# Kernel tuning notes

Hardware: AMD Instinct MI355X
Metric: run time of the kernel (lower is better)

Reference implementation:

```python
import jax, jax.numpy as jnp
import numpy as np

B, H, S, D = 2, 16, 1024, 64

def setup_inputs() -> dict:
    key = jax.random.key(0)
    k1, k2 = jax.random.split(key)
    # x1 is the output of a softmax (attention probabilities): non-negative, rows sum to 1
    logits = jax.random.normal(k1, (B, H, S, S), dtype=jnp.float32)
    x1 = jax.nn.softmax(logits, axis=-1)
    x2 = jax.random.normal(k2, (B, H, S, D), dtype=jnp.float32)
    return {"x1": x1, "x2": x2}

def reference(x1, x2):
    # Forward of EfficientMemoryGEMMWithSoftmax: exact batched GEMM.
    # (The outlier/low-bit compression only affects what is cached for backward;
    #  the forward output is the exact product.)
    return jnp.einsum('bhsk,bhkd->bhsd', x1, x2)
```

## Files before the change

kernel.cpp:

```cpp
#include <hip/hip_runtime.h>
#include <hip/hip_bf16.h>

typedef __attribute__((ext_vector_type(8))) short short8_t;
typedef __attribute__((ext_vector_type(4))) short short4_t;
typedef __attribute__((ext_vector_type(4))) float f32x4;

#define S_DIM   1024
#define D_DIM   64
#define BM      128
#define KC      64
#define NCHUNK  (S_DIM / KC)
#define BSTRIDE 72
#define THREADS 512

__device__ __forceinline__ ushort f2bf(float f) {
    __hip_bfloat16 h = __float2bfloat16(f);
    return __builtin_bit_cast(ushort, h);
}

#define SYNC() do { \
    __builtin_amdgcn_sched_barrier(0); \
    asm volatile("s_waitcnt lgkmcnt(0)"); \
    __builtin_amdgcn_s_barrier(); \
    __builtin_amdgcn_sched_barrier(0); \
} while (0)

__global__ __launch_bounds__(THREADS, 1)
void gemm_sm_kernel(const float* __restrict__ x1,
                    const float* __restrict__ x2,
                    float* __restrict__ out) {
    __shared__ ushort lds_b[2][D_DIM * BSTRIDE];

    const int tid = threadIdx.x;
    const int bid = blockIdx.x;
    const int batch   = (bid & 7) * 4 + (bid >> 6);
    const int rowtile = (bid >> 3) & 7;
    const int row0    = rowtile * BM;

    const float* Abase = x1 + (size_t)batch * (S_DIM * S_DIM) + (size_t)row0 * S_DIM;
    const float* Bbase = x2 + (size_t)batch * (S_DIM * D_DIM);
    float*       Cbase = out + (size_t)batch * (S_DIM * D_DIM) + (size_t)row0 * D_DIM;

    const int w = tid >> 6;
    const int l = tid & 63;
    const int fr = l & 15, fg = l >> 4;

    const float* arow = Abase + (size_t)(w * 16 + fr) * S_DIM + fg * 8;

    const int bd  = l;
    const int bk0 = w * 4;

    int bidx[4][2];
    #pragma unroll
    for (int nf = 0; nf < 4; ++nf) {
        const int col = nf * 16 + fr;
        #pragma unroll
        for (int ks = 0; ks < 2; ++ks)
            bidx[nf][ks] = col * BSTRIDE + ks * 32 + fg * 8;
    }

    float a0[16], a1[16], b0[8], b1[8];

    auto loadA = [&](int t, float (&A)[16]) {
        #pragma unroll
        for (int ks = 0; ks < 2; ++ks) {
            const float* p = arow + t * KC + ks * 32;
            float4 v0 = *reinterpret_cast<const float4*>(p);
            float4 v1 = *reinterpret_cast<const float4*>(p + 4);
            A[ks * 8 + 0] = v0.x; A[ks * 8 + 1] = v0.y;
            A[ks * 8 + 2] = v0.z; A[ks * 8 + 3] = v0.w;
            A[ks * 8 + 4] = v1.x; A[ks * 8 + 5] = v1.y;
            A[ks * 8 + 6] = v1.z; A[ks * 8 + 7] = v1.w;
        }
    };
    auto loadB = [&](int t, float (&B)[8]) {
        const float* bp = Bbase + (size_t)t * KC * D_DIM + bd;
        #pragma unroll
        for (int i = 0; i < 2; ++i)
            #pragma unroll
            for (int j = 0; j < 4; ++j)
                B[i * 4 + j] = bp[(bk0 + 32 * i + j) * D_DIM];
    };
    auto storeB = [&](ushort* lb, const float (&B)[8]) {
        #pragma unroll
        for (int i = 0; i < 2; ++i) {
            short4_t bv;
            #pragma unroll
            for (int j = 0; j < 4; ++j) bv[j] = (short)f2bf(B[i * 4 + j]);
            *reinterpret_cast<short4_t*>(&lb[bd * BSTRIDE + bk0 + 32 * i]) = bv;
        }
    };

    f32x4 acc[4];
    #pragma unroll
    for (int nf = 0; nf < 4; ++nf) acc[nf] = f32x4{0.f, 0.f, 0.f, 0.f};

    auto buildAF = [&](const float (&A)[16], short8_t (&af)[2]) {
        #pragma unroll
        for (int ks = 0; ks < 2; ++ks)
            #pragma unroll
            for (int j = 0; j < 8; ++j)
                af[ks][j] = (short)f2bf(A[ks * 8 + j]);
    };
    auto computeMFMA = [&](const short8_t (&af)[2], const ushort* lb) {
        #pragma unroll
        for (int nf = 0; nf < 4; ++nf) {
            #pragma unroll
            for (int ks = 0; ks < 2; ++ks) {
                short8_t bf = *reinterpret_cast<const short8_t*>(&lb[bidx[nf][ks]]);
                acc[nf] = __builtin_amdgcn_mfma_f32_16x16x32_bf16(
                    af[ks], bf, acc[nf], 0, 0, 0);
            }
        }
    };

    loadA(0, a0); loadB(0, b0);
    loadA(1, a1); loadB(1, b1);
    storeB(&lds_b[0][0], b0);
    SYNC();

    #pragma unroll 1
    for (int ti = 0; ti < NCHUNK; ti += 2) {
        {
            short8_t af[2];
            buildAF(a0, af);
            if (ti + 2 < NCHUNK) { loadA(ti + 2, a0); loadB(ti + 2, b0); }
            storeB(&lds_b[1][0], b1);
            computeMFMA(af, &lds_b[0][0]);
        }
        SYNC();
        {
            short8_t af[2];
            buildAF(a1, af);
            if (ti + 3 < NCHUNK) { loadA(ti + 3, a1); loadB(ti + 3, b1); }
            if (ti + 2 < NCHUNK) storeB(&lds_b[0][0], b0);
            computeMFMA(af, &lds_b[1][0]);
        }
        SYNC();
    }

    #pragma unroll
    for (int nf = 0; nf < 4; ++nf)
        #pragma unroll
        for (int j = 0; j < 4; ++j) {
            const int r = w * 16 + fg * 4 + j;
            const int c = nf * 16 + fr;
            Cbase[(size_t)r * D_DIM + c] = acc[nf][j];
        }
}

extern "C" void kernel_launch(void* const* d_in, const int* in_sizes, int n_in,
                              void* d_out, int out_size, void* d_ws, size_t ws_size,
                              hipStream_t stream) {
    const float* x1 = (const float*)d_in[0];
    const float* x2 = (const float*)d_in[1];
    float* out = (float*)d_out;
    dim3 grid(256), block(THREADS);
    gemm_sm_kernel<<<grid, block, 0, stream>>>(x1, x2, out);
}
```

Measured before the change: 31.26 us.

## Stage A through swizzled LDS with coalesced row loads and double K chunk

A is now loaded with fully coalesced float4 reads (32 threads per row), converted to bf16 and staged in an XOR-swizzled LDS double buffer, instead of each lane reading its own MFMA fragment directly from global memory. The K chunk grows from 64 to 128, halving the number of barriers, and the loop becomes a single-buffer-per-iteration prefetch pipeline. The cost is more LDS traffic and usage, plus extra register pressure from holding 8 float4 A values and 16 B values in flight.

New measurement: 27.75 us. 11.2% less time.

```diff
diff --git a/kernel.cpp b/kernel.cpp
--- a/kernel.cpp
+++ b/kernel.cpp
@@ -8,9 +8,9 @@
 #define S_DIM   1024
 #define D_DIM   64
 #define BM      128
-#define KC      64
+#define KC      128
 #define NCHUNK  (S_DIM / KC)
-#define BSTRIDE 72
+#define BSTRIDE 136
 #define THREADS 512
 
 __device__ __forceinline__ ushort f2bf(float f) {
@@ -29,6 +29,7 @@
 void gemm_sm_kernel(const float* __restrict__ x1,
                     const float* __restrict__ x2,
                     float* __restrict__ out) {
+    __shared__ ushort lds_a[2][BM * KC];
     __shared__ ushort lds_b[2][D_DIM * BSTRIDE];
 
     const int tid = threadIdx.x;
@@ -45,49 +46,59 @@
     const int l = tid & 63;
     const int fr = l & 15, fg = l >> 4;
 
-    const float* arow = Abase + (size_t)(w * 16 + fr) * S_DIM + fg * 8;
+    const int arow  = tid >> 5;
+    const int acol4 = (tid & 31) * 4;
+    const float* aptr = Abase + (size_t)arow * S_DIM + acol4;
+    const int aw_u16 = (arow * KC + acol4) ^ ((arow & 7) << 3);
 
     const int bd  = l;
     const int bk0 = w * 4;
 
-    int bidx[4][2];
+    int aidx[4];
+    {
+        const int row = w * 16 + fr;
+        #pragma unroll
+        for (int ks = 0; ks < 4; ++ks)
+            aidx[ks] = (row * KC + ks * 32 + fg * 8) ^ ((row & 7) << 3);
+    }
+    int bbase[4];
     #pragma unroll
-    for (int nf = 0; nf < 4; ++nf) {
-        const int col = nf * 16 + fr;
+    for (int nf = 0; nf < 4; ++nf)
+        bbase[nf] = (nf * 16 + fr) * BSTRIDE + fg * 8;
+
+    float4 Ar[8];
+    float  Br[16];
+
+    auto loadA = [&](int t) {
+        const float* p = aptr + t * KC;
         #pragma unroll
-        for (int ks = 0; ks < 2; ++ks)
-            bidx[nf][ks] = col * BSTRIDE + ks * 32 + fg * 8;
-    }
-
-    float a0[16], a1[16], b0[8], b1[8];
-
-    auto loadA = [&](int t, float (&A)[16]) {
+        for (int i = 0; i < 8; ++i)
+            Ar[i] = *reinterpret_cast<const float4*>(p + (size_t)i * 16 * S_DIM);
+    };
+    auto loadB = [&](int t) {
+        const float* bp = Bbase + (size_t)t * KC * D_DIM + bd;
         #pragma unroll
-        for (int ks = 0; ks < 2; ++ks) {
-            const float* p = arow + t * KC + ks * 32;
-            float4 v0 = *reinterpret_cast<const float4*>(p);
-            float4 v1 = *reinterpret_cast<const float4*>(p + 4);
-            A[ks * 8 + 0] = v0.x; A[ks * 8 + 1] = v0.y;
-            A[ks * 8 + 2] = v0.z; A[ks * 8 + 3] = v0.w;
-            A[ks * 8 + 4] = v1.x; A[ks * 8 + 5] = v1.y;
-            A[ks * 8 + 6] = v1.z; A[ks * 8 + 7] = v1.w;
+        for (int i = 0; i < 4; ++i)
+            #pragma unroll
+            for (int j = 0; j < 4; ++j)
+                Br[i * 4 + j] = bp[(size_t)(bk0 + i * 32 + j) * D_DIM];
+    };
+    auto storeA = [&](ushort* la) {
+        #pragma unroll
+        for (int i = 0; i < 8; ++i) {
+            short4_t v;
+            v[0] = (short)f2bf(Ar[i].x); v[1] = (short)f2bf(Ar[i].y);
+            v[2] = (short)f2bf(Ar[i].z); v[3] = (short)f2bf(Ar[i].w);
+            *reinterpret_cast<short4_t*>(&la[aw_u16 + i * 16 * KC]) = v;
         }
     };
-    auto loadB = [&](int t, float (&B)[8]) {
-        const float* bp = Bbase + (size_t)t * KC * D_DIM + bd;
+    auto storeB = [&](ushort* lb) {
         #pragma unroll
-        for (int i = 0; i < 2; ++i)
+        for (int i = 0; i < 4; ++i) {
+            short4_t v;
             #pragma unroll
-            for (int j = 0; j < 4; ++j)
-                B[i * 4 + j] = bp[(bk0 + 32 * i + j) * D_DIM];
-    };
-    auto storeB = [&](ushort* lb, const float (&B)[8]) {
-        #pragma unroll
-        for (int i = 0; i < 2; ++i) {
-            short4_t bv;
-            #pragma unroll
-            for (int j = 0; j < 4; ++j) bv[j] = (short)f2bf(B[i * 4 + j]);
-            *reinterpret_cast<short4_t*>(&lb[bd * BSTRIDE + bk0 + 32 * i]) = bv;
+            for (int j = 0; j < 4; ++j) v[j] = (short)f2bf(Br[i * 4 + j]);
+            *reinterpret_cast<short4_t*>(&lb[bd * BSTRIDE + bk0 + i * 32]) = v;
         }
     };
 
@@ -95,48 +106,36 @@
     #pragma unroll
     for (int nf = 0; nf < 4; ++nf) acc[nf] = f32x4{0.f, 0.f, 0.f, 0.f};
 
-    auto buildAF = [&](const float (&A)[16], short8_t (&af)[2]) {
+    auto compute = [&](const ushort* la, const ushort* lb) {
+        short8_t af[4];
         #pragma unroll
-        for (int ks = 0; ks < 2; ++ks)
+        for (int ks = 0; ks < 4; ++ks)
+            af[ks] = *reinterpret_cast<const short8_t*>(&la[aidx[ks]]);
+        #pragma unroll
+        for (int ks = 0; ks < 4; ++ks)
             #pragma unroll
-            for (int j = 0; j < 8; ++j)
-                af[ks][j] = (short)f2bf(A[ks * 8 + j]);
-    };
-    auto computeMFMA = [&](const short8_t (&af)[2], const ushort* lb) {
-        #pragma unroll
-        for (int nf = 0; nf < 4; ++nf) {
-            #pragma unroll
-            for (int ks = 0; ks < 2; ++ks) {
-                short8_t bf = *reinterpret_cast<const short8_t*>(&lb[bidx[nf][ks]]);
+            for (int nf = 0; nf < 4; ++nf) {
+                short8_t bf = *reinterpret_cast<const short8_t*>(&lb[bbase[nf] + ks * 32]);
                 acc[nf] = __builtin_amdgcn_mfma_f32_16x16x32_bf16(
                     af[ks], bf, acc[nf], 0, 0, 0);
             }
-        }
     };
 
-    loadA(0, a0); loadB(0, b0);
-    loadA(1, a1); loadB(1, b1);
-    storeB(&lds_b[0][0], b0);
+    loadA(0); loadB(0);
+    storeA(&lds_a[0][0]); storeB(&lds_b[0][0]);
     SYNC();
 
     #pragma unroll 1
-    for (int ti = 0; ti < NCHUNK; ti += 2) {
-        {
-            short8_t af[2];
-            buildAF(a0, af);
-            if (ti + 2 < NCHUNK) { loadA(ti + 2, a0); loadB(ti + 2, b0); }
-            storeB(&lds_b[1][0], b1);
-            computeMFMA(af, &lds_b[0][0]);
+    for (int t = 0; t < NCHUNK; ++t) {
+        if (t + 1 < NCHUNK) { loadA(t + 1); loadB(t + 1); }
+        __builtin_amdgcn_sched_barrier(0);
+        compute(&lds_a[t & 1][0], &lds_b[t & 1][0]);
+        __builtin_amdgcn_sched_barrier(0);
+        if (t + 1 < NCHUNK) {
+            storeA(&lds_a[(t + 1) & 1][0]);
+            storeB(&lds_b[(t + 1) & 1][0]);
+            SYNC();
         }
-        SYNC();
-        {
-            short8_t af[2];
-            buildAF(a1, af);
-            if (ti + 3 < NCHUNK) { loadA(ti + 3, a1); loadB(ti + 3, b1); }
-            if (ti + 2 < NCHUNK) storeB(&lds_b[0][0], b0);
-            computeMFMA(af, &lds_b[1][0]);
-        }
-        SYNC();
     }
 
     #pragma unroll
```

## Stream A tiles into swizzled LDS via async global_load_lds with 4-stage ring

Applied to the files above, without the earlier changes.

Replaces the register-staged loads of the fp32 A matrix with direct global-to-LDS loads into a 4-deep ring of swizzled LDS buffers, issued three chunks ahead. The B tile is re-laid out in LDS in MFMA-fragment order. The main loop becomes a single-chunk loop with one barrier per chunk. The aim is to deepen the memory pipeline for this bandwidth-bound GEMM and free registers. In exchange it uses about 144KB of LDS. Synchronisation relies on compiler vmcnt waits, and the barrier macro only waits on lgkmcnt, which risks reading LDS before the async loads land.

Result: slower. 32.14 us (+2.8%).

```diff
diff --git a/kernel.cpp b/kernel.cpp
--- a/kernel.cpp
+++ b/kernel.cpp
@@ -1,5 +1,6 @@
 #include <hip/hip_runtime.h>
 #include <hip/hip_bf16.h>
+#include <stdint.h>
 
 typedef __attribute__((ext_vector_type(8))) short short8_t;
 typedef __attribute__((ext_vector_type(4))) short short4_t;
@@ -10,8 +11,11 @@
 #define BM      128
 #define KC      64
 #define NCHUNK  (S_DIM / KC)
-#define BSTRIDE 72
 #define THREADS 512
+#define NBUF    4
+
+typedef const __attribute__((address_space(1))) uint32_t g_u32;
+typedef __attribute__((address_space(3))) uint32_t l_u32;
 
 __device__ __forceinline__ ushort f2bf(float f) {
     __hip_bfloat16 h = __float2bfloat16(f);
@@ -29,7 +33,8 @@
 void gemm_sm_kernel(const float* __restrict__ x1,
                     const float* __restrict__ x2,
                     float* __restrict__ out) {
-    __shared__ ushort lds_b[2][D_DIM * BSTRIDE];
+    __shared__ float  lds_a[NBUF][BM * KC];
+    __shared__ ushort lds_b[2][8 * 512];
 
     const int tid = threadIdx.x;
     const int bid = blockIdx.x;
@@ -45,34 +50,20 @@
     const int l = tid & 63;
     const int fr = l & 15, fg = l >> 4;
 
-    const float* arow = Abase + (size_t)(w * 16 + fr) * S_DIM + fg * 8;
+    auto gllA = [&](int t, int buf) {
+        #pragma unroll
+        for (int i = 0; i < 4; ++i) {
+            const int r  = w * 16 + i * 4 + (l >> 4);
+            const int kk = ((l & 15) * 4) ^ ((r & 7) << 3);
+            const float* src = Abase + (size_t)r * S_DIM + t * KC + kk;
+            float* dst = &lds_a[buf][w * 1024 + i * 256];
+            __builtin_amdgcn_global_load_lds((g_u32*)src, (l_u32*)dst, 16, 0, 0);
+        }
+    };
 
     const int bd  = l;
     const int bk0 = w * 4;
 
-    int bidx[4][2];
-    #pragma unroll
-    for (int nf = 0; nf < 4; ++nf) {
-        const int col = nf * 16 + fr;
-        #pragma unroll
-        for (int ks = 0; ks < 2; ++ks)
-            bidx[nf][ks] = col * BSTRIDE + ks * 32 + fg * 8;
-    }
-
-    float a0[16], a1[16], b0[8], b1[8];
-
-    auto loadA = [&](int t, float (&A)[16]) {
-        #pragma unroll
-        for (int ks = 0; ks < 2; ++ks) {
-            const float* p = arow + t * KC + ks * 32;
-            float4 v0 = *reinterpret_cast<const float4*>(p);
-            float4 v1 = *reinterpret_cast<const float4*>(p + 4);
-            A[ks * 8 + 0] = v0.x; A[ks * 8 + 1] = v0.y;
-            A[ks * 8 + 2] = v0.z; A[ks * 8 + 3] = v0.w;
-            A[ks * 8 + 4] = v1.x; A[ks * 8 + 5] = v1.y;
-            A[ks * 8 + 6] = v1.z; A[ks * 8 + 7] = v1.w;
-        }
-    };
     auto loadB = [&](int t, float (&B)[8]) {
         const float* bp = Bbase + (size_t)t * KC * D_DIM + bd;
         #pragma unroll
@@ -82,12 +73,15 @@
                 B[i * 4 + j] = bp[(bk0 + 32 * i + j) * D_DIM];
     };
     auto storeB = [&](ushort* lb, const float (&B)[8]) {
+        const int lfrag16 = (((w >> 1) << 4) | (l & 15)) * 16;
         #pragma unroll
         for (int i = 0; i < 2; ++i) {
-            short4_t bv;
+            const int f = i * 4 + (l >> 4);
+            const int byteoff = f * 1024 + ((lfrag16 + f * 32) & 1023) + (w & 1) * 8;
+            short4_t v;
             #pragma unroll
-            for (int j = 0; j < 4; ++j) bv[j] = (short)f2bf(B[i * 4 + j]);
-            *reinterpret_cast<short4_t*>(&lb[bd * BSTRIDE + bk0 + 32 * i]) = bv;
+            for (int j = 0; j < 4; ++j) v[j] = (short)f2bf(B[i * 4 + j]);
+            *reinterpret_cast<short4_t*>((char*)lb + byteoff) = v;
         }
     };
 
@@ -95,48 +89,57 @@
     #pragma unroll
     for (int nf = 0; nf < 4; ++nf) acc[nf] = f32x4{0.f, 0.f, 0.f, 0.f};
 
-    auto buildAF = [&](const float (&A)[16], short8_t (&af)[2]) {
+    int abase[2];
+    {
+        const int row = w * 16 + fr;
+        #pragma unroll
+        for (int ks = 0; ks < 2; ++ks)
+            abase[ks] = row * 64 + ((ks * 32 + fg * 8) ^ ((row & 7) << 3));
+    }
+
+    auto computeC = [&](const float* la, const ushort* lb) {
+        short8_t af[2];
+        #pragma unroll
+        for (int ks = 0; ks < 2; ++ks) {
+            f32x4 lo = *reinterpret_cast<const f32x4*>(&la[abase[ks]]);
+            f32x4 hi = *reinterpret_cast<const f32x4*>(&la[abase[ks] + 4]);
+            #pragma unroll
+            for (int j = 0; j < 4; ++j) {
+                af[ks][j]     = (short)f2bf(lo[j]);
+                af[ks][4 + j] = (short)f2bf(hi[j]);
+            }
+        }
         #pragma unroll
         for (int ks = 0; ks < 2; ++ks)
             #pragma unroll
-            for (int j = 0; j < 8; ++j)
-                af[ks][j] = (short)f2bf(A[ks * 8 + j]);
-    };
-    auto computeMFMA = [&](const short8_t (&af)[2], const ushort* lb) {
-        #pragma unroll
-        for (int nf = 0; nf < 4; ++nf) {
-            #pragma unroll
-            for (int ks = 0; ks < 2; ++ks) {
-                short8_t bf = *reinterpret_cast<const short8_t*>(&lb[bidx[nf][ks]]);
+            for (int nf = 0; nf < 4; ++nf) {
+                const int f = ks * 4 + nf;
+                const int byteoff = f * 1024 + ((l * 16 + f * 32) & 1023);
+                short8_t bf = *reinterpret_cast<const short8_t*>(
+                    (const char*)lb + byteoff);
                 acc[nf] = __builtin_amdgcn_mfma_f32_16x16x32_bf16(
                     af[ks], bf, acc[nf], 0, 0, 0);
             }
-        }
     };
 
-    loadA(0, a0); loadB(0, b0);
-    loadA(1, a1); loadB(1, b1);
+    float b0[8], b1[8];
+
+    gllA(0, 0); gllA(1, 1); gllA(2, 2);
+    loadB(0, b0); loadB(1, b1);
     storeB(&lds_b[0][0], b0);
     SYNC();
 
     #pragma unroll 1
-    for (int ti = 0; ti < NCHUNK; ti += 2) {
-        {
-            short8_t af[2];
-            buildAF(a0, af);
-            if (ti + 2 < NCHUNK) { loadA(ti + 2, a0); loadB(ti + 2, b0); }
-            storeB(&lds_b[1][0], b1);
-            computeMFMA(af, &lds_b[0][0]);
+    for (int t = 0; t < NCHUNK; ++t) {
+        const int pe = t & 1;
+        if (t + 3 < NCHUNK) gllA(t + 3, (t + 3) & 3);
+        if (t + 2 < NCHUNK) loadB(t + 2, pe ? b1 : b0);
+        __builtin_amdgcn_sched_barrier(0);
+        computeC(&lds_a[t & 3][0], &lds_b[pe][0]);
+        if (t + 1 < NCHUNK) {
+            storeB(&lds_b[pe ^ 1][0], pe ? b0 : b1);
+            SYNC();
         }
-        SYNC();
-        {
-            short8_t af[2];
-            buildAF(a1, af);
-            if (ti + 3 < NCHUNK) { loadA(ti + 3, a1); loadB(ti + 3, b1); }
-            if (ti + 2 < NCHUNK) storeB(&lds_b[0][0], b0);
-            computeMFMA(af, &lds_b[1][0]);
-        }
-        SYNC();
     }
 
     #pragma unroll
```
